# Kernel tuning notes

Hardware: AMD Instinct MI355X
Metric: run time of the kernel (lower is better)

Reference implementation:

```python
import jax, jax.numpy as jnp
import numpy as np

N_HEAD = 16
D_HEAD = 64  # d_model=1024 // n_head=16


def setup_inputs() -> dict:
    key = jax.random.key(0)
    ks = jax.random.split(key, 8)
    B, S, D = 2, 2048, 1024
    scale = 1.0 / np.sqrt(D)
    return {
        "q": jax.random.normal(ks[0], (B, S, D), jnp.float32),
        "k": jax.random.normal(ks[1], (B, S, D), jnp.float32),
        "v": jax.random.normal(ks[2], (B, S, D), jnp.float32),
        "w_q": jax.random.normal(ks[3], (D, D), jnp.float32) * scale,
        "w_k": jax.random.normal(ks[4], (D, D), jnp.float32) * scale,
        "w_v": jax.random.normal(ks[5], (D, D), jnp.float32) * scale,
        "w_fc": jax.random.normal(ks[6], (D, D), jnp.float32) * scale,
        "b_fc": jnp.zeros((D,), jnp.float32),
    }


def reference(q, k, v, w_q, w_k, w_v, w_fc, b_fc):
    B, Sq, D = q.shape
    # projections (torch Linear: x @ W.T), split into heads -> [B, H, S, Dh]
    def proj(x, w):
        return (x @ w.T).reshape(B, x.shape[1], N_HEAD, D_HEAD).transpose(0, 2, 1, 3)
    qh, kh, vh = proj(q, w_q), proj(k, w_k), proj(v, w_v)
    # scaled dot-product attention with explicit weights (dropout = identity, eval mode)
    scores = jnp.einsum("bhqd,bhkd->bhqk", qh, kh) / jnp.sqrt(jnp.float32(D_HEAD))
    attn = jax.nn.softmax(scores, axis=-1)  # [B, H, Sq, Sk]
    ctx = jnp.einsum("bhqk,bhkd->bhqd", attn, vh)
    ctx = ctx.transpose(0, 2, 1, 3).reshape(B, Sq, D)
    out = ctx @ w_fc.T + b_fc
    return out, attn
```

## Files before the change

### kernel.cpp

```cpp
#include <hip/hip_runtime.h>


using f16   = _Float16;
using f16x4 = __attribute__((ext_vector_type(4))) f16;
using f16x8 = __attribute__((ext_vector_type(8))) f16;
using f32x4 = __attribute__((ext_vector_type(4))) float;

#define MFMA16(a, b, c) __builtin_amdgcn_mfma_f32_16x16x32_f16((a), (b), (c), 0, 0, 0)

__device__ static inline float fexp2(float x) {
#if __has_builtin(__builtin_amdgcn_exp2f)
  return __builtin_amdgcn_exp2f(x);
#else
  return exp2f(x);
#endif
}

#define C1 0.18033688011112042f

#define WAIT_BARRIER(IMM)                                              \
  do {                                                                 \
    asm volatile("s_waitcnt vmcnt(" #IMM ") lgkmcnt(0)" ::: "memory"); \
    __builtin_amdgcn_s_barrier();                                      \
  } while (0)

__device__ static inline void gld16(const void* gptr, void* lptr) {
  __builtin_amdgcn_global_load_lds(
      (const __attribute__((address_space(1))) void*)gptr,
      (__attribute__((address_space(3))) void*)lptr, 16, 0, 0);
}

__device__ static inline unsigned int pack2(float a, float b) {
  union { f16 h[2]; unsigned int u; } x;
  x.h[0] = (f16)a; x.h[1] = (f16)b;
  return x.u;
}

__global__ __launch_bounds__(256) void cast_all(
    const float* __restrict__ q, const float* __restrict__ k,
    const float* __restrict__ v, const float* __restrict__ wq,
    const float* __restrict__ wk, const float* __restrict__ wv,
    const float* __restrict__ wfc, f16* __restrict__ ws) {
  int i = blockIdx.x * 256 + threadIdx.x;
  const float* src;
  f16* dst;
  int li;
  if (i < 3145728) {
    if (i < 1048576)      { src = q; dst = ws;            li = i; }
    else if (i < 2097152) { src = k; dst = ws + 4194304;  li = i - 1048576; }
    else                  { src = v; dst = ws + 8388608;  li = i - 2097152; }
  } else {
    int j = i - 3145728;
    int wsel = j >> 18;
    src = (wsel == 0) ? wq : (wsel == 1) ? wk : (wsel == 2) ? wv : wfc;
    dst = ws + 12582912 + wsel * 1048576;
    li = j & 262143;
  }
  float4 x = ((const float4*)src)[li];
  f16x4 y;
  y[0] = (f16)x.x; y[1] = (f16)x.y; y[2] = (f16)x.z; y[3] = (f16)x.w;
  ((f16x4*)dst)[li] = y;
}

template <int MODE, int BN>
__global__ __launch_bounds__(256) void gemm_bt(
    const f16* __restrict__ A0, const f16* __restrict__ W0,
    const float* __restrict__ bias, void* __restrict__ Cout) {
  constexpr int FJ = BN / 32;
  __shared__ unsigned short XA[8192];
  __shared__ unsigned short WB[BN * 64];
  int tid = threadIdx.x;
  int w = tid >> 6, l = tid & 63, lq = l & 15, g = l >> 4;
  int nb3 = blockIdx.x * BN, mb = blockIdx.y * 128;
  int wsel = (MODE == 4) ? (nb3 >> 10) : 0;
  int nb = (MODE == 4) ? (nb3 & 1023) : nb3;
  const f16* A = (MODE == 4) ? A0 + (size_t)wsel * 4194304 : A0;
  const f16* W = (MODE == 4) ? W0 + (size_t)wsel * 1048576 : W0;
  bool swapR = (MODE == 4) && (wsel == 2);
  int wi = w >> 1, wj = w & 1;

  f32x4 acc[4][FJ];
#pragma unroll
  for (int i = 0; i < 4; i++)
#pragma unroll
    for (int j = 0; j < FJ; j++) acc[i][j] = (f32x4){0.f, 0.f, 0.f, 0.f};

  char* Xb = (char*)XA;
  char* Wb = (char*)WB;
  int row = tid >> 3;
  int c = (tid & 7) ^ (row & 7);
  const f16* Asrc = A + (size_t)(mb + row) * 1024 + c * 8;
  const f16* Wsrc = W + (size_t)(nb + row) * 1024 + c * 8;

  for (int k0 = 0; k0 < 1024; k0 += 64) {
#pragma unroll
    for (int i2 = 0; i2 < 4; i2++)
      gld16(Asrc + k0 + i2 * 32 * 1024, Xb + i2 * 4096 + w * 1024);
#pragma unroll
    for (int i2 = 0; i2 < BN / 32; i2++)
      gld16(Wsrc + k0 + i2 * 32 * 1024, Wb + i2 * 4096 + w * 1024);
    __syncthreads();

    const char* at = swapR ? Wb : Xb;
    const char* bt = swapR ? Xb : Wb;

    f16x8 bfr[FJ][2];
#pragma unroll
    for (int f = 0; f < FJ; f++) {
      int r = wj * (BN / 2) + f * 16 + lq;
      int sw = (r & 7) << 4;
      bfr[f][0] = *(const f16x8*)(bt + r * 128 + ((g * 16) ^ sw));
      bfr[f][1] = *(const f16x8*)(bt + r * 128 + ((64 + g * 16) ^ sw));
    }
#pragma unroll
    for (int fi = 0; fi < 4; fi++) {
      int r = wi * 64 + fi * 16 + lq;
      int sw = (r & 7) << 4;
      f16x8 a0 = *(const f16x8*)(at + r * 128 + ((g * 16) ^ sw));
      f16x8 a1 = *(const f16x8*)(at + r * 128 + ((64 + g * 16) ^ sw));
#pragma unroll
      for (int fj = 0; fj < FJ; fj++) {
        acc[fi][fj] = MFMA16(a0, bfr[fj][0], acc[fi][fj]);
        acc[fi][fj] = MFMA16(a1, bfr[fj][1], acc[fi][fj]);
      }
    }
    __syncthreads();
  }

#pragma unroll
  for (int fi = 0; fi < 4; fi++) {
#pragma unroll
    for (int fj = 0; fj < FJ; fj++) {
#pragma unroll
      for (int jj = 0; jj < 4; jj++) {
        float v = acc[fi][fj][jj];
        int iG = (swapR ? nb : mb) + wi * 64 + fi * 16 + g * 4 + jj;
        int jG = (swapR ? mb : nb) + wj * (BN / 2) + fj * 16 + lq;
        if constexpr (MODE == 3) {
          int m2 = iG, n2 = jG;
          ((float*)Cout)[(size_t)m2 * 1024 + n2] = v + bias[n2];
        } else {
          f16* dstb = (f16*)Cout + (size_t)wsel * 4194304;
          if (!swapR) {
            int m2 = iG, n2 = jG;
            size_t dst = (size_t)((m2 >> 11) * 16 + (n2 >> 6)) * 131072 +
                         (size_t)(m2 & 2047) * 64 + (n2 & 63);
            dstb[dst] = (f16)v;
          } else {
            int n2 = iG, m2 = jG;
            size_t dst = (size_t)((m2 >> 11) * 1024 + n2) * 2048 + (m2 & 2047);
            dstb[dst] = (f16)v;
          }
        }
      }
    }
  }
}

__global__ __launch_bounds__(256, 2) void attn_fused(
    const f16* __restrict__ qh, const f16* __restrict__ kh,
    const f16* __restrict__ vt, float* __restrict__ attn,
    f16* __restrict__ ctx) {
  __shared__ unsigned short Kl0[4096], Kl1[4096];
  __shared__ unsigned short Vl0[4096], Vl1[4096];
  __shared__ unsigned short Pl[8192];
  int tid = threadIdx.x;
  int w = tid >> 6, l = tid & 63, lq = l & 15, g = l >> 4;

  int bid = blockIdx.x;
  int xcd = bid & 7, j = bid >> 3;
  int bh = xcd * 4 + (j >> 4);
  int qt = j & 15;

  const f16* qbase = qh + (size_t)(bh * 2048 + qt * 128 + w * 32 + lq) * 64;
  f16x8 qf[2][2];
#pragma unroll
  for (int f = 0; f < 2; f++) {
    qf[f][0] = *(const f16x8*)(qbase + f * 16 * 64 + g * 8);
    qf[f][1] = *(const f16x8*)(qbase + f * 16 * 64 + 32 + g * 8);
  }

  char* Kb0 = (char*)Kl0;
  char* Kb1 = (char*)Kl1;
  char* Vb0 = (char*)Vl0;
  char* Vb1 = (char*)Vl1;
  char* Pw  = (char*)Pl + w * 4096;

  int row = tid >> 3;
  int c = (tid & 7) ^ (row & 7);
  const f16* ksrc = kh + (size_t)bh * 2048 * 64 + (size_t)row * 64 + c * 8;
  const f16* vsrc = vt + (size_t)bh * 64 * 2048 + (size_t)row * 2048 + c * 8;

  int swq = (lq & 7) << 4;

  float ls[2] = {0.f, 0.f};
  gld16(ksrc,           Kb0 + w * 1024);
  gld16(ksrc + 32 * 64, Kb0 + 4096 + w * 1024);
  WAIT_BARRIER(0);
  for (int t = 0; t < 32; t++) {
    char* KbC = (t & 1) ? Kb1 : Kb0;
    char* KbN = (t & 1) ? Kb0 : Kb1;
    if (t < 31) {
      const f16* kp = ksrc + (size_t)(t + 1) * 4096;
      gld16(kp,           KbN + w * 1024);
      gld16(kp + 32 * 64, KbN + 4096 + w * 1024);
    }
#pragma unroll
    for (int cf = 0; cf < 4; cf++) {
      int kr = cf * 16 + lq;
      int sw = (kr & 7) << 4;
      f16x8 ka  = *(const f16x8*)(KbC + kr * 128 + ((g * 16) ^ sw));
      f16x8 kb2 = *(const f16x8*)(KbC + kr * 128 + ((64 + g * 16) ^ sw));
#pragma unroll
      for (int f = 0; f < 2; f++) {
        f32x4 s = (f32x4){0.f, 0.f, 0.f, 0.f};
        s = MFMA16(ka, qf[f][0], s);
        s = MFMA16(kb2, qf[f][1], s);
        ls[f] += fexp2(s[0] * C1) + fexp2(s[1] * C1) +
                 fexp2(s[2] * C1) + fexp2(s[3] * C1);
      }
    }
    WAIT_BARRIER(0);
  }
  float linv[2];
#pragma unroll
  for (int f = 0; f < 2; f++) {
    float t = ls[f];
    t += __shfl_xor(t, 16);
    t += __shfl_xor(t, 32);
    linv[f] = 1.0f / t;
  }

  f32x4 acc[2][4];
#pragma unroll
  for (int f = 0; f < 2; f++)
#pragma unroll
    for (int i = 0; i < 4; i++) acc[f][i] = (f32x4){0.f, 0.f, 0.f, 0.f};

  float* attnrow0 =
      attn + ((size_t)bh * 2048 + qt * 128 + w * 32 + lq) * 2048;
  float* attnrow1 = attnrow0 + 16 * 2048;

  gld16(ksrc,             Kb0 + w * 1024);
  gld16(ksrc + 32 * 64,   Kb0 + 4096 + w * 1024);
  gld16(vsrc,             Vb0 + w * 1024);
  gld16(vsrc + 32 * 2048, Vb0 + 4096 + w * 1024);
  WAIT_BARRIER(0);
  for (int t = 0; t < 32; t++) {
    int kt = t * 64;
    char* KbC = (t & 1) ? Kb1 : Kb0;
    char* KbN = (t & 1) ? Kb0 : Kb1;
    char* VbC = (t & 1) ? Vb1 : Vb0;
    char* VbN = (t & 1) ? Vb0 : Vb1;
    if (t < 31) {
      const f16* kp = ksrc + (size_t)(t + 1) * 4096;
      const f16* vp = vsrc + (size_t)(t + 1) * 64;
      gld16(kp,             KbN + w * 1024);
      gld16(kp + 32 * 64,   KbN + 4096 + w * 1024);
      gld16(vp,             VbN + w * 1024);
      gld16(vp + 32 * 2048, VbN + 4096 + w * 1024);
    }

#pragma unroll
    for (int cf = 0; cf < 4; cf++) {
      int kr = cf * 16 + lq;
      int sw = (kr & 7) << 4;
      f16x8 ka  = *(const f16x8*)(KbC + kr * 128 + ((g * 16) ^ sw));
      f16x8 kb2 = *(const f16x8*)(KbC + kr * 128 + ((64 + g * 16) ^ sw));
      int k0 = cf * 16 + g * 4;
#pragma unroll
      for (int f = 0; f < 2; f++) {
        f32x4 s = (f32x4){0.f, 0.f, 0.f, 0.f};
        s = MFMA16(ka, qf[f][0], s);
        s = MFMA16(kb2, qf[f][1], s);
        float e0 = fexp2(s[0] * C1) * linv[f];
        float e1 = fexp2(s[1] * C1) * linv[f];
        float e2 = fexp2(s[2] * C1) * linv[f];
        float e3 = fexp2(s[3] * C1) * linv[f];
        float4 o = {e0, e1, e2, e3};
        *(float4*)((f ? attnrow1 : attnrow0) + kt + cf * 16 + g * 4) = o;
        char* Pr = Pw + (f * 16 + lq) * 128;
        *(unsigned int*)(Pr + ((k0 * 2) ^ swq))       = pack2(e0, e1);
        *(unsigned int*)(Pr + (((k0 + 2) * 2) ^ swq)) = pack2(e2, e3);
      }
    }

    {
      f16x8 pb[2][2];
#pragma unroll
      for (int f = 0; f < 2; f++) {
        char* Pr = Pw + (f * 16 + lq) * 128;
        pb[f][0] = *(const f16x8*)(Pr + ((g * 16) ^ swq));
        pb[f][1] = *(const f16x8*)(Pr + ((64 + g * 16) ^ swq));
      }
#pragma unroll
      for (int af = 0; af < 4; af++) {
        int vr = af * 16 + lq;
        int sv = (vr & 7) << 4;
        f16x8 va0 = *(const f16x8*)(VbC + vr * 128 + ((g * 16) ^ sv));
        f16x8 va1 = *(const f16x8*)(VbC + vr * 128 + ((64 + g * 16) ^ sv));
#pragma unroll
        for (int f = 0; f < 2; f++) {
          acc[f][af] = MFMA16(va0, pb[f][0], acc[f][af]);
          acc[f][af] = MFMA16(va1, pb[f][1], acc[f][af]);
        }
      }
    }
    WAIT_BARRIER(8);
  }

#pragma unroll
  for (int f = 0; f < 2; f++) {
    char* Pr = Pw + (f * 16 + lq) * 128;
#pragma unroll
    for (int af = 0; af < 4; af++) {
#pragma unroll
      for (int jj = 0; jj < 4; jj += 2) {
        int dh0 = af * 16 + g * 4 + jj;
        *(unsigned int*)(Pr + ((dh0 * 2) ^ swq)) =
            pack2(acc[f][af][jj], acc[f][af][jj + 1]);
      }
    }
  }
  {
    int q2 = l >> 1, cc = l & 1;
    int swr = (q2 & 7) << 4;
    int b = bh >> 4, h = bh & 15;
    f16* crow =
        ctx + ((size_t)b * 2048 + qt * 128 + w * 32 + q2) * 1024 + h * 64;
#pragma unroll
    for (int t2 = 0; t2 < 4; t2++) {
      f16x8 v2 = *(const f16x8*)(Pw + q2 * 128 + ((cc * 64 + t2 * 16) ^ swr));
      *(f16x8*)(crow + cc * 32 + t2 * 8) = v2;
    }
  }
}

extern "C" void kernel_launch(void* const* d_in, const int* in_sizes, int n_in,
                              void* d_out, int out_size, void* d_ws,
                              size_t ws_size, hipStream_t stream) {
  (void)in_sizes; (void)n_in; (void)out_size; (void)ws_size;
  const float* q   = (const float*)d_in[0];
  const float* k   = (const float*)d_in[1];
  const float* v   = (const float*)d_in[2];
  const float* wq  = (const float*)d_in[3];
  const float* wk  = (const float*)d_in[4];
  const float* wv  = (const float*)d_in[5];
  const float* wfc = (const float*)d_in[6];
  const float* bfc = (const float*)d_in[7];

  f16* ws = (f16*)d_ws;
  f16* qf   = ws;
  f16* wqf  = ws + 12582912;
  f16* wfcf = ws + 15728640;
  f16* qhp  = ws + 16777216;
  f16* khp  = ws + 20971520;
  f16* vtp  = ws + 25165824;
  f16* ctxp = ws + 29360128;

  float* outp  = (float*)d_out;
  float* attnp = outp + 4194304;

  cast_all<<<16384, 256, 0, stream>>>(q, k, v, wq, wk, wv, wfc, ws);
  gemm_bt<4, 128><<<dim3(24, 32), 256, 0, stream>>>(qf, wqf, nullptr, qhp);
  attn_fused<<<512, 256, 0, stream>>>(qhp, khp, vtp, attnp, ctxp);
  gemm_bt<3, 64><<<dim3(16, 32), 256, 0, stream>>>(ctxp, wfcf, bfc, outp);
}
```

Before: 282.0 us.

## Read K/V directly from global memory and drop LDS double-buffering and barriers

Removes the shared-memory double-buffered staging of K and V tiles, which used async global-to-LDS loads and block barriers. Each wave now loads its K and V fragments straight from global memory into registers, relying on L1/L2 caching, so the per-tile barriers go away. It also makes the attention-probability writes nontemporal stores and drops the min-blocks launch bound. The risks are redundant global traffic, since each of the four waves now fetches the same K/V data, and exposed load latency without prefetch.

Result: slower. 385.2 us (+36.6%).

```diff
diff --git a/kernel.cpp b/kernel.cpp
--- a/kernel.cpp
+++ b/kernel.cpp
@@ -17,12 +17,6 @@
 }
 
 #define C1 0.18033688011112042f
-
-#define WAIT_BARRIER(IMM)                                              \
-  do {                                                                 \
-    asm volatile("s_waitcnt vmcnt(" #IMM ") lgkmcnt(0)" ::: "memory"); \
-    __builtin_amdgcn_s_barrier();                                      \
-  } while (0)
 
 __device__ static inline void gld16(const void* gptr, void* lptr) {
   __builtin_amdgcn_global_load_lds(
@@ -157,12 +151,10 @@
   }
 }
 
-__global__ __launch_bounds__(256, 2) void attn_fused(
+__global__ __launch_bounds__(256) void attn_fused(
     const f16* __restrict__ qh, const f16* __restrict__ kh,
     const f16* __restrict__ vt, float* __restrict__ attn,
     f16* __restrict__ ctx) {
-  __shared__ unsigned short Kl0[4096], Kl1[4096];
-  __shared__ unsigned short Vl0[4096], Vl1[4096];
   __shared__ unsigned short Pl[8192];
   int tid = threadIdx.x;
   int w = tid >> 6, l = tid & 63, lq = l & 15, g = l >> 4;
@@ -180,37 +172,19 @@
     qf[f][1] = *(const f16x8*)(qbase + f * 16 * 64 + 32 + g * 8);
   }
 
-  char* Kb0 = (char*)Kl0;
-  char* Kb1 = (char*)Kl1;
-  char* Vb0 = (char*)Vl0;
-  char* Vb1 = (char*)Vl1;
-  char* Pw  = (char*)Pl + w * 4096;
-
-  int row = tid >> 3;
-  int c = (tid & 7) ^ (row & 7);
-  const f16* ksrc = kh + (size_t)bh * 2048 * 64 + (size_t)row * 64 + c * 8;
-  const f16* vsrc = vt + (size_t)bh * 64 * 2048 + (size_t)row * 2048 + c * 8;
-
+  char* Pw = (char*)Pl + w * 4096;
+  const f16* kbh = kh + (size_t)bh * 2048 * 64;
+  const f16* vbh = vt + (size_t)bh * 64 * 2048;
   int swq = (lq & 7) << 4;
 
   float ls[2] = {0.f, 0.f};
-  gld16(ksrc,           Kb0 + w * 1024);
-  gld16(ksrc + 32 * 64, Kb0 + 4096 + w * 1024);
-  WAIT_BARRIER(0);
   for (int t = 0; t < 32; t++) {
-    char* KbC = (t & 1) ? Kb1 : Kb0;
-    char* KbN = (t & 1) ? Kb0 : Kb1;
-    if (t < 31) {
-      const f16* kp = ksrc + (size_t)(t + 1) * 4096;
-      gld16(kp,           KbN + w * 1024);
-      gld16(kp + 32 * 64, KbN + 4096 + w * 1024);
-    }
+    const f16* kp = kbh + (size_t)t * 4096 + (size_t)lq * 64 + g * 8;
 #pragma unroll
     for (int cf = 0; cf < 4; cf++) {
-      int kr = cf * 16 + lq;
-      int sw = (kr & 7) << 4;
-      f16x8 ka  = *(const f16x8*)(KbC + kr * 128 + ((g * 16) ^ sw));
-      f16x8 kb2 = *(const f16x8*)(KbC + kr * 128 + ((64 + g * 16) ^ sw));
+      const f16* kr = kp + cf * 1024;
+      f16x8 ka  = *(const f16x8*)(kr);
+      f16x8 kb2 = *(const f16x8*)(kr + 32);
 #pragma unroll
       for (int f = 0; f < 2; f++) {
         f32x4 s = (f32x4){0.f, 0.f, 0.f, 0.f};
@@ -220,7 +194,6 @@
                  fexp2(s[2] * C1) + fexp2(s[3] * C1);
       }
     }
-    WAIT_BARRIER(0);
   }
   float linv[2];
 #pragma unroll
@@ -241,32 +214,14 @@
       attn + ((size_t)bh * 2048 + qt * 128 + w * 32 + lq) * 2048;
   float* attnrow1 = attnrow0 + 16 * 2048;
 
-  gld16(ksrc,             Kb0 + w * 1024);
-  gld16(ksrc + 32 * 64,   Kb0 + 4096 + w * 1024);
-  gld16(vsrc,             Vb0 + w * 1024);
-  gld16(vsrc + 32 * 2048, Vb0 + 4096 + w * 1024);
-  WAIT_BARRIER(0);
   for (int t = 0; t < 32; t++) {
     int kt = t * 64;
-    char* KbC = (t & 1) ? Kb1 : Kb0;
-    char* KbN = (t & 1) ? Kb0 : Kb1;
-    char* VbC = (t & 1) ? Vb1 : Vb0;
-    char* VbN = (t & 1) ? Vb0 : Vb1;
-    if (t < 31) {
-      const f16* kp = ksrc + (size_t)(t + 1) * 4096;
-      const f16* vp = vsrc + (size_t)(t + 1) * 64;
-      gld16(kp,             KbN + w * 1024);
-      gld16(kp + 32 * 64,   KbN + 4096 + w * 1024);
-      gld16(vp,             VbN + w * 1024);
-      gld16(vp + 32 * 2048, VbN + 4096 + w * 1024);
-    }
 
 #pragma unroll
     for (int cf = 0; cf < 4; cf++) {
-      int kr = cf * 16 + lq;
-      int sw = (kr & 7) << 4;
-      f16x8 ka  = *(const f16x8*)(KbC + kr * 128 + ((g * 16) ^ sw));
-      f16x8 kb2 = *(const f16x8*)(KbC + kr * 128 + ((64 + g * 16) ^ sw));
+      const f16* kr = kbh + (size_t)(kt + cf * 16 + lq) * 64 + g * 8;
+      f16x8 ka  = *(const f16x8*)(kr);
+      f16x8 kb2 = *(const f16x8*)(kr + 32);
       int k0 = cf * 16 + g * 4;
 #pragma unroll
       for (int f = 0; f < 2; f++) {
@@ -277,8 +232,9 @@
         float e1 = fexp2(s[1] * C1) * linv[f];
         float e2 = fexp2(s[2] * C1) * linv[f];
         float e3 = fexp2(s[3] * C1) * linv[f];
-        float4 o = {e0, e1, e2, e3};
-        *(float4*)((f ? attnrow1 : attnrow0) + kt + cf * 16 + g * 4) = o;
+        f32x4 o = {e0, e1, e2, e3};
+        __builtin_nontemporal_store(
+            o, (f32x4*)((f ? attnrow1 : attnrow0) + kt + cf * 16 + g * 4));
         char* Pr = Pw + (f * 16 + lq) * 128;
         *(unsigned int*)(Pr + ((k0 * 2) ^ swq))       = pack2(e0, e1);
         *(unsigned int*)(Pr + (((k0 + 2) * 2) ^ swq)) = pack2(e2, e3);
@@ -295,10 +251,9 @@
       }
 #pragma unroll
       for (int af = 0; af < 4; af++) {
-        int vr = af * 16 + lq;
-        int sv = (vr & 7) << 4;
-        f16x8 va0 = *(const f16x8*)(VbC + vr * 128 + ((g * 16) ^ sv));
-        f16x8 va1 = *(const f16x8*)(VbC + vr * 128 + ((64 + g * 16) ^ sv));
+        const f16* vr = vbh + (size_t)(af * 16 + lq) * 2048 + kt + g * 8;
+        f16x8 va0 = *(const f16x8*)(vr);
+        f16x8 va1 = *(const f16x8*)(vr + 32);
 #pragma unroll
         for (int f = 0; f < 2; f++) {
           acc[f][af] = MFMA16(va0, pb[f][0], acc[f][af]);
@@ -306,7 +261,6 @@
         }
       }
     }
-    WAIT_BARRIER(8);
   }
 
 #pragma unroll
```
